# Performance work log

Hardware: AMD Instinct MI355X
Metric: run time of the kernel (lower is better)

The kernel has to match this reference:

```python
import jax, jax.numpy as jnp
import numpy as np

FP8_MAX = 448.0  # torch.finfo(float8_e4m3fn).max
TINY = float(np.finfo(np.float32).tiny)
BN = BK = 128  # block sizes


def _make_fp8_weight(key, N, K):
    """Mirror _create_fp8_weight: per-128x128-block scales, fp8 quantized values."""
    w = jax.random.normal(key, (N, K), jnp.float32) * 0.01
    wb = w.reshape(N // BN, BN, K // BK, BK)
    amax = jnp.abs(wb).max(axis=(1, 3))
    scale_inv = jnp.maximum(amax / FP8_MAX, TINY)  # [N/BN, K/BK]
    wq = (wb / scale_inv[:, None, :, None]).reshape(N, K)
    wq = wq.astype(jnp.float8_e4m3fn).astype(jnp.float32)  # fp8-rounded values
    return wq, scale_inv


def _dequant(wq, scale_inv):
    N, K = wq.shape
    nb, kb = scale_inv.shape
    wb = wq.reshape(nb, N // nb, kb, K // kb) * scale_inv[:, None, :, None]
    return wb.reshape(N, K)


def setup_inputs() -> dict:
    key = jax.random.key(0)
    kx, k1, k2, k3 = jax.random.split(key, 4)
    T, H, F = 4096, 2048, 7168  # tokens, hidden_dim, ffn_dim
    x = jax.random.normal(kx, (T, H), jnp.float32)
    w1_q, w1_s = _make_fp8_weight(k1, F, H)
    w3_q, w3_s = _make_fp8_weight(k3, F, H)
    w2_q, w2_s = _make_fp8_weight(k2, H, F)
    return {"hidden_states": x, "w1_q": w1_q, "w1_s": w1_s,
            "w3_q": w3_q, "w3_s": w3_s, "w2_q": w2_q, "w2_s": w2_s}


def reference(hidden_states, w1_q, w1_s, w3_q, w3_s, w2_q, w2_s):
    x = hidden_states
    w1 = _dequant(w1_q, w1_s)  # [F, H]
    w3 = _dequant(w3_q, w3_s)  # [F, H]
    w2 = _dequant(w2_q, w2_s)  # [H, F]
    g = x @ w1.T               # [T, F]
    u = x @ w3.T               # [T, F]
    fused = jax.nn.silu(g) * u
    return fused @ w2.T        # [T, H]
```

## Files before the change

### kernel.cpp

```cpp
#include <hip/hip_runtime.h>
#include <stdint.h>

typedef __attribute__((ext_vector_type(8))) short short8;
typedef __attribute__((ext_vector_type(4))) float floatx4;

__device__ __forceinline__ unsigned short f2bf(float f) {
  union { float f; unsigned int u; } c; c.f = f;
  unsigned int u = c.u;
  unsigned int r = (u + 0x7fffu + ((u >> 16) & 1u)) >> 16;
  return (unsigned short)r;
}
__device__ __forceinline__ float bf2f(unsigned short h) {
  union { unsigned int u; float f; } c; c.u = ((unsigned int)h) << 16;
  return c.f;
}

__device__ __forceinline__ void load16_to_lds(const void* g, void* l) {
  __builtin_amdgcn_global_load_lds(
      (const __attribute__((address_space(1))) unsigned int*)g,
      (__attribute__((address_space(3))) unsigned int*)l, 16, 0, 0);
}

__global__ void f32_to_bf16_kernel(const float* __restrict__ in,
                                   unsigned short* __restrict__ out, long n4) {
  long i = blockIdx.x * (long)blockDim.x + threadIdx.x;
  if (i >= n4) return;
  float4 v = ((const float4*)in)[i];
  ushort4 o;
  o.x = f2bf(v.x); o.y = f2bf(v.y); o.z = f2bf(v.z); o.w = f2bf(v.w);
  ((ushort4*)out)[i] = o;
}

__global__ void dequant2_kernel(const float* __restrict__ w1q,
                                const float* __restrict__ s1,
                                const float* __restrict__ w3q,
                                const float* __restrict__ s3,
                                unsigned short* __restrict__ o1,
                                unsigned short* __restrict__ o3,
                                int K, int sK) {
  int n = blockIdx.y;
  int k = blockIdx.x * 1024 + threadIdx.x * 4;
  size_t idx = (size_t)n * K + k;
  int sidx = (n >> 7) * sK + (k >> 7);
  float sc1 = s1[sidx], sc3 = s3[sidx];
  float4 v1 = *(const float4*)(w1q + idx);
  float4 v3 = *(const float4*)(w3q + idx);
  ushort4 a, b;
  a.x = f2bf(v1.x * sc1); a.y = f2bf(v1.y * sc1);
  a.z = f2bf(v1.z * sc1); a.w = f2bf(v1.w * sc1);
  b.x = f2bf(v3.x * sc3); b.y = f2bf(v3.y * sc3);
  b.z = f2bf(v3.z * sc3); b.w = f2bf(v3.w * sc3);
  *(ushort4*)(o1 + idx) = a;
  *(ushort4*)(o3 + idx) = b;
}

__global__ void dequant1_kernel(const float* __restrict__ wq,
                                const float* __restrict__ s,
                                unsigned short* __restrict__ out,
                                int K, int sK) {
  int n = blockIdx.y;
  int k = blockIdx.x * 1024 + threadIdx.x * 4;
  size_t idx = (size_t)n * K + k;
  float sc = s[(n >> 7) * sK + (k >> 7)];
  float4 v = *(const float4*)(wq + idx);
  ushort4 o;
  o.x = f2bf(v.x * sc); o.y = f2bf(v.y * sc);
  o.z = f2bf(v.z * sc); o.w = f2bf(v.w * sc);
  *(ushort4*)(out + idx) = o;
}


__global__ __launch_bounds__(512, 4) void dual_gemm_silu(
    const unsigned short* __restrict__ A,
    const unsigned short* __restrict__ B1,
    const unsigned short* __restrict__ B3,
    unsigned short* __restrict__ C,
    int M, int N, int K) {
  __shared__ unsigned short As[128 * 64];
  __shared__ unsigned short B1s[128 * 64];
  __shared__ unsigned short B3s[128 * 64];

  const int tid = threadIdx.x;
  const int lane = tid & 63;
  const int wave = tid >> 6;
  const int wm = wave >> 2;
  const int wn = wave & 3;
  const int m0 = blockIdx.y * 128, n0 = blockIdx.x * 128;

  const int s0 = tid, s1 = tid + 512;
  const int r0 = s0 >> 3, c0 = ((s0 & 7) ^ (r0 & 7)) * 8;
  const int r1 = s1 >> 3, c1 = ((s1 & 7) ^ (r1 & 7)) * 8;

  const int q = lane >> 4;
  const int r16 = lane & 15;
  const int rx = r16 & 7;

  floatx4 acc_g[4][2], acc_u[4][2];
#pragma unroll
  for (int i = 0; i < 4; i++)
#pragma unroll
    for (int j = 0; j < 2; j++) {
      acc_g[i][j] = (floatx4){0.f, 0.f, 0.f, 0.f};
      acc_u[i][j] = (floatx4){0.f, 0.f, 0.f, 0.f};
    }

  const unsigned short* ag0 = A + (size_t)(m0 + r0) * K + c0;
  const unsigned short* ag1 = A + (size_t)(m0 + r1) * K + c1;
  const unsigned short* b1g0 = B1 + (size_t)(n0 + r0) * K + c0;
  const unsigned short* b1g1 = B1 + (size_t)(n0 + r1) * K + c1;
  const unsigned short* b3g0 = B3 + (size_t)(n0 + r0) * K + c0;
  const unsigned short* b3g1 = B3 + (size_t)(n0 + r1) * K + c1;

  for (int k0 = 0; k0 < K; k0 += 64) {
    load16_to_lds(ag0 + k0, &As[s0 * 8]);
    load16_to_lds(ag1 + k0, &As[s1 * 8]);
    load16_to_lds(b1g0 + k0, &B1s[s0 * 8]);
    load16_to_lds(b1g1 + k0, &B1s[s1 * 8]);
    load16_to_lds(b3g0 + k0, &B3s[s0 * 8]);
    load16_to_lds(b3g1 + k0, &B3s[s1 * 8]);
    __syncthreads();

#pragma unroll
    for (int kh = 0; kh < 2; kh++) {
      const int kq = kh * 4 + q;
      short8 a[4], b1v[2], b3v[2];
#pragma unroll
      for (int t = 0; t < 4; t++) {
        int row = wm * 64 + t * 16 + r16;
        a[t] = *(const short8*)&As[(row * 8 + (kq ^ rx)) * 8];
      }
#pragma unroll
      for (int j = 0; j < 2; j++) {
        int row = wn * 32 + j * 16 + r16;
        int u = (row * 8 + (kq ^ rx)) * 8;
        b1v[j] = *(const short8*)&B1s[u];
        b3v[j] = *(const short8*)&B3s[u];
      }
#pragma unroll
      for (int i = 0; i < 4; i++)
#pragma unroll
        for (int j = 0; j < 2; j++) {
          acc_g[i][j] = __builtin_amdgcn_mfma_f32_16x16x32_bf16(
              a[i], b1v[j], acc_g[i][j], 0, 0, 0);
          acc_u[i][j] = __builtin_amdgcn_mfma_f32_16x16x32_bf16(
              a[i], b3v[j], acc_u[i][j], 0, 0, 0);
        }
    }
    __syncthreads();
  }

#pragma unroll
  for (int i = 0; i < 4; i++) {
    int row0 = m0 + wm * 64 + i * 16 + q * 4;
#pragma unroll
    for (int j = 0; j < 2; j++) {
      int col = n0 + wn * 32 + j * 16 + r16;
#pragma unroll
      for (int rr = 0; rr < 4; rr++) {
        float gv = acc_g[i][j][rr];
        float uv = acc_u[i][j][rr];
        float sv = gv / (1.f + __expf(-gv)) * uv;
        C[(size_t)(row0 + rr) * N + col] = f2bf(sv);
      }
    }
  }
}

__global__ __launch_bounds__(256, 2) void gemm_nt_f32_sk(
    const unsigned short* __restrict__ A,
    const unsigned short* __restrict__ B,
    float* __restrict__ C,
    int M, int N, int K) {
  __shared__ unsigned short As[128 * 64];
  __shared__ unsigned short Bs[128 * 64];

  const int tid = threadIdx.x;
  const int lane = tid & 63;
  const int wave = tid >> 6;
  const int wm = wave >> 1;
  const int wn = wave & 1;
  const int m0 = blockIdx.y * 128, n0 = blockIdx.x * 128;
  const int kbase = blockIdx.z * (K >> 1);
  const int kend = kbase + (K >> 1);

  int soff[4], sdst[4];
#pragma unroll
  for (int p = 0; p < 4; p++) {
    int u = tid + 256 * p;
    int r = u >> 3;
    int c = ((u & 7) ^ (r & 7)) * 8;
    soff[p] = r * K + c;
    sdst[p] = u * 8;
  }

  const int q = lane >> 4;
  const int r16 = lane & 15;
  const int rx = r16 & 7;

  floatx4 acc[4][4];
#pragma unroll
  for (int i = 0; i < 4; i++)
#pragma unroll
    for (int j = 0; j < 4; j++) acc[i][j] = (floatx4){0.f, 0.f, 0.f, 0.f};

  const unsigned short* Abase = A + (size_t)m0 * K;
  const unsigned short* Bbase = B + (size_t)n0 * K;

  for (int k0 = kbase; k0 < kend; k0 += 64) {
#pragma unroll
    for (int p = 0; p < 4; p++) {
      load16_to_lds(Abase + soff[p] + k0, &As[sdst[p]]);
      load16_to_lds(Bbase + soff[p] + k0, &Bs[sdst[p]]);
    }
    __syncthreads();

#pragma unroll
    for (int kh = 0; kh < 2; kh++) {
      const int kq = kh * 4 + q;
      short8 a[4], b[4];
#pragma unroll
      for (int t = 0; t < 4; t++) {
        int row = wm * 64 + t * 16 + r16;
        a[t] = *(const short8*)&As[(row * 8 + (kq ^ rx)) * 8];
      }
#pragma unroll
      for (int j = 0; j < 4; j++) {
        int row = wn * 64 + j * 16 + r16;
        b[j] = *(const short8*)&Bs[(row * 8 + (kq ^ rx)) * 8];
      }
#pragma unroll
      for (int i = 0; i < 4; i++)
#pragma unroll
        for (int j = 0; j < 4; j++)
          acc[i][j] = __builtin_amdgcn_mfma_f32_16x16x32_bf16(
              a[i], b[j], acc[i][j], 0, 0, 0);
    }
    __syncthreads();
  }

#pragma unroll
  for (int i = 0; i < 4; i++) {
    int row0 = m0 + wm * 64 + i * 16 + q * 4;
#pragma unroll
    for (int j = 0; j < 4; j++) {
      int col = n0 + wn * 64 + j * 16 + r16;
#pragma unroll
      for (int rr = 0; rr < 4; rr++)
        unsafeAtomicAdd(&C[(size_t)(row0 + rr) * N + col], acc[i][j][rr]);
    }
  }
}

extern "C" void kernel_launch(void* const* d_in, const int* in_sizes, int n_in,
                              void* d_out, int out_size, void* d_ws, size_t ws_size,
                              hipStream_t stream) {
  const float* x = (const float*)d_in[0];
  const float* w1q = (const float*)d_in[1];
  const float* w1s = (const float*)d_in[2];
  const float* w3q = (const float*)d_in[3];
  const float* w3s = (const float*)d_in[4];
  const float* w2q = (const float*)d_in[5];
  const float* w2s = (const float*)d_in[6];

  const int T = 4096, H = 2048, F = 7168;

  char* ws = (char*)d_ws;
  unsigned short* xb  = (unsigned short*)ws;  ws += (size_t)T * H * 2;
  unsigned short* w1b = (unsigned short*)ws;  ws += (size_t)F * H * 2;
  unsigned short* w3b = (unsigned short*)ws;  ws += (size_t)F * H * 2;
  unsigned short* w2b = (unsigned short*)ws;  ws += (size_t)H * F * 2;
  unsigned short* g   = (unsigned short*)ws;  ws += (size_t)T * F * 2;

  long xn4 = (long)T * H / 4;

  f32_to_bf16_kernel<<<(xn4 + 255) / 256, 256, 0, stream>>>(x, xb, xn4);
  dequant2_kernel<<<dim3(H / 1024, F), 256, 0, stream>>>(
      w1q, w1s, w3q, w3s, w1b, w3b, H, H / 128);
  dequant1_kernel<<<dim3(F / 1024, H), 256, 0, stream>>>(
      w2q, w2s, w2b, F, F / 128);

  dual_gemm_silu<<<dim3(F / 128, T / 128), 512, 0, stream>>>(xb, w1b, w3b, g, T, F, H);

  hipMemsetAsync(d_out, 0, (size_t)T * H * 4, stream);
  gemm_nt_f32_sk<<<dim3(H / 128, T / 128, 2), 256, 0, stream>>>(
      g, w2b, (float*)d_out, T, H, F);
}
```

Baseline: 582.9 us.

## Double-buffer LDS in both GEMMs and fuse preprocessing into one kernel

Both GEMM kernels switch from a single 64-wide K tile with two barriers per step to two 32-wide K buffers. The next tile's global-to-LDS load is issued before computing on the current one, with one barrier per iteration, so memory latency can overlap the MFMA work. The swizzle changes to match the 4-chunk row layout. The three conversion and dequant kernels merge into one launch, and the second GEMM's launch bounds ask for 3 blocks per CU. The smaller K step doubles the number of barriers and loop iterations, and higher occupancy pressure may cap registers.

```diff
diff --git a/kernel.cpp b/kernel.cpp
--- a/kernel.cpp
+++ b/kernel.cpp
@@ -10,10 +10,6 @@
   unsigned int r = (u + 0x7fffu + ((u >> 16) & 1u)) >> 16;
   return (unsigned short)r;
 }
-__device__ __forceinline__ float bf2f(unsigned short h) {
-  union { unsigned int u; float f; } c; c.u = ((unsigned int)h) << 16;
-  return c.f;
-}
 
 __device__ __forceinline__ void load16_to_lds(const void* g, void* l) {
   __builtin_amdgcn_global_load_lds(
@@ -21,52 +17,53 @@
       (__attribute__((address_space(3))) unsigned int*)l, 16, 0, 0);
 }
 
-__global__ void f32_to_bf16_kernel(const float* __restrict__ in,
-                                   unsigned short* __restrict__ out, long n4) {
-  long i = blockIdx.x * (long)blockDim.x + threadIdx.x;
-  if (i >= n4) return;
-  float4 v = ((const float4*)in)[i];
-  ushort4 o;
-  o.x = f2bf(v.x); o.y = f2bf(v.y); o.z = f2bf(v.z); o.w = f2bf(v.w);
-  ((ushort4*)out)[i] = o;
-}
-
-__global__ void dequant2_kernel(const float* __restrict__ w1q,
-                                const float* __restrict__ s1,
-                                const float* __restrict__ w3q,
-                                const float* __restrict__ s3,
-                                unsigned short* __restrict__ o1,
-                                unsigned short* __restrict__ o3,
-                                int K, int sK) {
-  int n = blockIdx.y;
-  int k = blockIdx.x * 1024 + threadIdx.x * 4;
-  size_t idx = (size_t)n * K + k;
-  int sidx = (n >> 7) * sK + (k >> 7);
-  float sc1 = s1[sidx], sc3 = s3[sidx];
-  float4 v1 = *(const float4*)(w1q + idx);
-  float4 v3 = *(const float4*)(w3q + idx);
-  ushort4 a, b;
-  a.x = f2bf(v1.x * sc1); a.y = f2bf(v1.y * sc1);
-  a.z = f2bf(v1.z * sc1); a.w = f2bf(v1.w * sc1);
-  b.x = f2bf(v3.x * sc3); b.y = f2bf(v3.y * sc3);
-  b.z = f2bf(v3.z * sc3); b.w = f2bf(v3.w * sc3);
-  *(ushort4*)(o1 + idx) = a;
-  *(ushort4*)(o3 + idx) = b;
-}
-
-__global__ void dequant1_kernel(const float* __restrict__ wq,
-                                const float* __restrict__ s,
-                                unsigned short* __restrict__ out,
-                                int K, int sK) {
-  int n = blockIdx.y;
-  int k = blockIdx.x * 1024 + threadIdx.x * 4;
-  size_t idx = (size_t)n * K + k;
-  float sc = s[(n >> 7) * sK + (k >> 7)];
-  float4 v = *(const float4*)(wq + idx);
-  ushort4 o;
-  o.x = f2bf(v.x * sc); o.y = f2bf(v.y * sc);
-  o.z = f2bf(v.z * sc); o.w = f2bf(v.w * sc);
-  *(ushort4*)(out + idx) = o;
+__global__ void preproc_kernel(const float* __restrict__ x,
+                               unsigned short* __restrict__ xb,
+                               const float* __restrict__ w1q,
+                               const float* __restrict__ s1,
+                               unsigned short* __restrict__ w1b,
+                               const float* __restrict__ w3q,
+                               const float* __restrict__ s3,
+                               unsigned short* __restrict__ w3b,
+                               const float* __restrict__ w2q,
+                               const float* __restrict__ s2,
+                               unsigned short* __restrict__ w2b) {
+  const int bid = blockIdx.x;
+  const int tid = threadIdx.x;
+  if (bid < 14336) {
+    int n = bid >> 1;
+    int k = (bid & 1) * 1024 + tid * 4;
+    size_t idx = (size_t)n * 2048 + k;
+    int sidx = (n >> 7) * 16 + (k >> 7);
+    float sc1 = s1[sidx], sc3 = s3[sidx];
+    float4 v1 = *(const float4*)(w1q + idx);
+    float4 v3 = *(const float4*)(w3q + idx);
+    ushort4 a, b;
+    a.x = f2bf(v1.x * sc1); a.y = f2bf(v1.y * sc1);
+    a.z = f2bf(v1.z * sc1); a.w = f2bf(v1.w * sc1);
+    b.x = f2bf(v3.x * sc3); b.y = f2bf(v3.y * sc3);
+    b.z = f2bf(v3.z * sc3); b.w = f2bf(v3.w * sc3);
+    *(ushort4*)(w1b + idx) = a;
+    *(ushort4*)(w3b + idx) = b;
+  } else if (bid < 28672) {
+    int b = bid - 14336;
+    int n = b / 7;
+    int kb = b - n * 7;
+    int k = kb * 1024 + tid * 4;
+    size_t idx = (size_t)n * 7168 + k;
+    float sc = s2[(n >> 7) * 56 + (k >> 7)];
+    float4 v = *(const float4*)(w2q + idx);
+    ushort4 o;
+    o.x = f2bf(v.x * sc); o.y = f2bf(v.y * sc);
+    o.z = f2bf(v.z * sc); o.w = f2bf(v.w * sc);
+    *(ushort4*)(w2b + idx) = o;
+  } else {
+    size_t i = (size_t)(bid - 28672) * 256 + tid;
+    float4 v = ((const float4*)x)[i];
+    ushort4 o;
+    o.x = f2bf(v.x); o.y = f2bf(v.y); o.z = f2bf(v.z); o.w = f2bf(v.w);
+    ((ushort4*)xb)[i] = o;
+  }
 }
 
 
@@ -76,9 +73,9 @@
     const unsigned short* __restrict__ B3,
     unsigned short* __restrict__ C,
     int M, int N, int K) {
-  __shared__ unsigned short As[128 * 64];
-  __shared__ unsigned short B1s[128 * 64];
-  __shared__ unsigned short B3s[128 * 64];
+  __shared__ unsigned short As[2][128 * 32];
+  __shared__ unsigned short B1s[2][128 * 32];
+  __shared__ unsigned short B3s[2][128 * 32];
 
   const int tid = threadIdx.x;
   const int lane = tid & 63;
@@ -87,13 +84,16 @@
   const int wn = wave & 3;
   const int m0 = blockIdx.y * 128, n0 = blockIdx.x * 128;
 
-  const int s0 = tid, s1 = tid + 512;
-  const int r0 = s0 >> 3, c0 = ((s0 & 7) ^ (r0 & 7)) * 8;
-  const int r1 = s1 >> 3, c1 = ((s1 & 7) ^ (r1 & 7)) * 8;
+  const int sr = tid >> 2;
+  const int sc = ((tid & 3) ^ (sr & 3)) * 8;
+  const int ldst = tid * 8;
+  const unsigned short* ag = A + (size_t)(m0 + sr) * K + sc;
+  const unsigned short* b1g = B1 + (size_t)(n0 + sr) * K + sc;
+  const unsigned short* b3g = B3 + (size_t)(n0 + sr) * K + sc;
 
   const int q = lane >> 4;
   const int r16 = lane & 15;
-  const int rx = r16 & 7;
+  const int rq = r16 & 3;
 
   floatx4 acc_g[4][2], acc_u[4][2];
 #pragma unroll
@@ -104,49 +104,48 @@
       acc_u[i][j] = (floatx4){0.f, 0.f, 0.f, 0.f};
     }
 
-  const unsigned short* ag0 = A + (size_t)(m0 + r0) * K + c0;
-  const unsigned short* ag1 = A + (size_t)(m0 + r1) * K + c1;
-  const unsigned short* b1g0 = B1 + (size_t)(n0 + r0) * K + c0;
-  const unsigned short* b1g1 = B1 + (size_t)(n0 + r1) * K + c1;
-  const unsigned short* b3g0 = B3 + (size_t)(n0 + r0) * K + c0;
-  const unsigned short* b3g1 = B3 + (size_t)(n0 + r1) * K + c1;
-
-  for (int k0 = 0; k0 < K; k0 += 64) {
-    load16_to_lds(ag0 + k0, &As[s0 * 8]);
-    load16_to_lds(ag1 + k0, &As[s1 * 8]);
-    load16_to_lds(b1g0 + k0, &B1s[s0 * 8]);
-    load16_to_lds(b1g1 + k0, &B1s[s1 * 8]);
-    load16_to_lds(b3g0 + k0, &B3s[s0 * 8]);
-    load16_to_lds(b3g1 + k0, &B3s[s1 * 8]);
+  int aoffs[4], boffs[2];
+#pragma unroll
+  for (int t = 0; t < 4; t++)
+    aoffs[t] = ((wm * 64 + t * 16 + r16) * 4 + (q ^ rq)) * 8;
+#pragma unroll
+  for (int j = 0; j < 2; j++)
+    boffs[j] = ((wn * 32 + j * 16 + r16) * 4 + (q ^ rq)) * 8;
+
+  const int nIter = K >> 5;
+
+  load16_to_lds(ag, &As[0][ldst]);
+  load16_to_lds(b1g, &B1s[0][ldst]);
+  load16_to_lds(b3g, &B3s[0][ldst]);
+
+  for (int it = 0; it < nIter; ++it) {
     __syncthreads();
-
-#pragma unroll
-    for (int kh = 0; kh < 2; kh++) {
-      const int kq = kh * 4 + q;
-      short8 a[4], b1v[2], b3v[2];
-#pragma unroll
-      for (int t = 0; t < 4; t++) {
-        int row = wm * 64 + t * 16 + r16;
-        a[t] = *(const short8*)&As[(row * 8 + (kq ^ rx)) * 8];
+    const int c = it & 1;
+    if (it + 1 < nIter) {
+      const int k0 = (it + 1) << 5;
+      const int nc = c ^ 1;
+      load16_to_lds(ag + k0, &As[nc][ldst]);
+      load16_to_lds(b1g + k0, &B1s[nc][ldst]);
+      load16_to_lds(b3g + k0, &B3s[nc][ldst]);
+    }
+    short8 a[4], b1v[2], b3v[2];
+#pragma unroll
+    for (int t = 0; t < 4; t++)
+      a[t] = *(const short8*)&As[c][aoffs[t]];
+#pragma unroll
+    for (int j = 0; j < 2; j++) {
+      b1v[j] = *(const short8*)&B1s[c][boffs[j]];
+      b3v[j] = *(const short8*)&B3s[c][boffs[j]];
+    }
+#pragma unroll
+    for (int i = 0; i < 4; i++)
+#pragma unroll
+      for (int j = 0; j < 2; j++) {
+        acc_g[i][j] = __builtin_amdgcn_mfma_f32_16x16x32_bf16(
+            a[i], b1v[j], acc_g[i][j], 0, 0, 0);
+        acc_u[i][j] = __builtin_amdgcn_mfma_f32_16x16x32_bf16(
+            a[i], b3v[j], acc_u[i][j], 0, 0, 0);
       }
-#pragma unroll
-      for (int j = 0; j < 2; j++) {
-        int row = wn * 32 + j * 16 + r16;
-        int u = (row * 8 + (kq ^ rx)) * 8;
-        b1v[j] = *(const short8*)&B1s[u];
-        b3v[j] = *(const short8*)&B3s[u];
-      }
-#pragma unroll
-      for (int i = 0; i < 4; i++)
-#pragma unroll
-        for (int j = 0; j < 2; j++) {
-          acc_g[i][j] = __builtin_amdgcn_mfma_f32_16x16x32_bf16(
-              a[i], b1v[j], acc_g[i][j], 0, 0, 0);
-          acc_u[i][j] = __builtin_amdgcn_mfma_f32_16x16x32_bf16(
-              a[i], b3v[j], acc_u[i][j], 0, 0, 0);
-        }
-    }
-    __syncthreads();
   }
 
 #pragma unroll
@@ -166,13 +165,13 @@
   }
 }
 
-__global__ __launch_bounds__(256, 2) void gemm_nt_f32_sk(
+__global__ __launch_bounds__(256, 3) void gemm_nt_f32_sk(
     const unsigned short* __restrict__ A,
     const unsigned short* __restrict__ B,
     float* __restrict__ C,
     int M, int N, int K) {
-  __shared__ unsigned short As[128 * 64];
-  __shared__ unsigned short Bs[128 * 64];
+  __shared__ unsigned short As[2][128 * 32];
+  __shared__ unsigned short Bs[2][128 * 32];
 
   const int tid = threadIdx.x;
   const int lane = tid & 63;
@@ -181,21 +180,21 @@
   const int wn = wave & 1;
   const int m0 = blockIdx.y * 128, n0 = blockIdx.x * 128;
   const int kbase = blockIdx.z * (K >> 1);
-  const int kend = kbase + (K >> 1);
-
-  int soff[4], sdst[4];
-#pragma unroll
-  for (int p = 0; p < 4; p++) {
+  const int nIter = K >> 6;
+
+  int soff[2], sdst[2];
+#pragma unroll
+  for (int p = 0; p < 2; p++) {
     int u = tid + 256 * p;
-    int r = u >> 3;
-    int c = ((u & 7) ^ (r & 7)) * 8;
+    int r = u >> 2;
+    int c = ((u & 3) ^ (r & 3)) * 8;
     soff[p] = r * K + c;
     sdst[p] = u * 8;
   }
 
   const int q = lane >> 4;
   const int r16 = lane & 15;
-  const int rx = r16 & 7;
+  const int rq = r16 & 3;
 
   floatx4 acc[4][4];
 #pragma unroll
@@ -203,39 +202,46 @@
 #pragma unroll
     for (int j = 0; j < 4; j++) acc[i][j] = (floatx4){0.f, 0.f, 0.f, 0.f};
 
-  const unsigned short* Abase = A + (size_t)m0 * K;
-  const unsigned short* Bbase = B + (size_t)n0 * K;
-
-  for (int k0 = kbase; k0 < kend; k0 += 64) {
-#pragma unroll
-    for (int p = 0; p < 4; p++) {
-      load16_to_lds(Abase + soff[p] + k0, &As[sdst[p]]);
-      load16_to_lds(Bbase + soff[p] + k0, &Bs[sdst[p]]);
-    }
+  int aoffs[4], boffs[4];
+#pragma unroll
+  for (int t = 0; t < 4; t++) {
+    aoffs[t] = ((wm * 64 + t * 16 + r16) * 4 + (q ^ rq)) * 8;
+    boffs[t] = ((wn * 64 + t * 16 + r16) * 4 + (q ^ rq)) * 8;
+  }
+
+  const unsigned short* Abase = A + (size_t)m0 * K + kbase;
+  const unsigned short* Bbase = B + (size_t)n0 * K + kbase;
+
+#pragma unroll
+  for (int p = 0; p < 2; p++) {
+    load16_to_lds(Abase + soff[p], &As[0][sdst[p]]);
+    load16_to_lds(Bbase + soff[p], &Bs[0][sdst[p]]);
+  }
+
+  for (int it = 0; it < nIter; ++it) {
     __syncthreads();
-
-#pragma unroll
-    for (int kh = 0; kh < 2; kh++) {
-      const int kq = kh * 4 + q;
-      short8 a[4], b[4];
-#pragma unroll
-      for (int t = 0; t < 4; t++) {
-        int row = wm * 64 + t * 16 + r16;
-        a[t] = *(const short8*)&As[(row * 8 + (kq ^ rx)) * 8];
+    const int c = it & 1;
+    if (it + 1 < nIter) {
+      const int k0 = (it + 1) << 5;
+      const int nc = c ^ 1;
+#pragma unroll
+      for (int p = 0; p < 2; p++) {
+        load16_to_lds(Abase + soff[p] + k0, &As[nc][sdst[p]]);
+        load16_to_lds(Bbase + soff[p] + k0, &Bs[nc][sdst[p]]);
       }
-#pragma unroll
-      for (int j = 0; j < 4; j++) {
-        int row = wn * 64 + j * 16 + r16;
-        b[j] = *(const short8*)&Bs[(row * 8 + (kq ^ rx)) * 8];
-      }
-#pragma unroll
-      for (int i = 0; i < 4; i++)
-#pragma unroll
-        for (int j = 0; j < 4; j++)
-          acc[i][j] = __builtin_amdgcn_mfma_f32_16x16x32_bf16(
-              a[i], b[j], acc[i][j], 0, 0, 0);
-    }
-    __syncthreads();
+    }
+    short8 a[4], b[4];
+#pragma unroll
+    for (int t = 0; t < 4; t++) {
+      a[t] = *(const short8*)&As[c][aoffs[t]];
+      b[t] = *(const short8*)&Bs[c][boffs[t]];
+    }
+#pragma unroll
+    for (int i = 0; i < 4; i++)
+#pragma unroll
+      for (int j = 0; j < 4; j++)
+        acc[i][j] = __builtin_amdgcn_mfma_f32_16x16x32_bf16(
+            a[i], b[j], acc[i][j], 0, 0, 0);
   }
 
 #pragma unroll
@@ -271,13 +277,8 @@
   unsigned short* w2b = (unsigned short*)ws;  ws += (size_t)H * F * 2;
   unsigned short* g   = (unsigned short*)ws;  ws += (size_t)T * F * 2;
 
-  long xn4 = (long)T * H / 4;
-
-  f32_to_bf16_kernel<<<(xn4 + 255) / 256, 256, 0, stream>>>(x, xb, xn4);
-  dequant2_kernel<<<dim3(H / 1024, F), 256, 0, stream>>>(
-      w1q, w1s, w3q, w3s, w1b, w3b, H, H / 128);
-  dequant1_kernel<<<dim3(F / 1024, H), 256, 0, stream>>>(
-      w2q, w2s, w2b, F, F / 128);
+  preproc_kernel<<<36864, 256, 0, stream>>>(
+      x, xb, w1q, w1s, w1b, w3q, w3s, w3b, w2q, w2s, w2b);
 
   dual_gemm_silu<<<dim3(F / 128, T / 128), 512, 0, stream>>>(xb, w1b, w3b, g, T, F, H);
 
```

Measured after the change: 664.1 us. 1.14x slower.
